# Kernel tuning notes

Measured on AMD Instinct MI355X. Metric: run time of the kernel, lower is better.

## Reference

```python
import jax, jax.numpy as jnp
import numpy as np
import math

NHID = 32
FEAT_SIZE = 32
FEAT_SIZE_LIST = [16, 32, 32, 32]
SEQ_LEN = len(FEAT_SIZE_LIST)   # 4
N_EDGE_LABELS = 3
NLAYERS = 2
N_GRAPHS = 64
FINAL = SEQ_LEN * NHID          # 128


def _pos_enc(max_len, dim):
    pe = np.zeros((max_len, dim), dtype=np.float32)
    pos = np.arange(max_len, dtype=np.float32)[:, None]
    div = np.exp(np.arange(0, dim, 2, dtype=np.float32) * (-math.log(10000.0) / dim))
    pe[:, 0::2] = np.sin(pos * div)
    pe[:, 1::2] = np.cos(pos * div)
    return jnp.asarray(pe)


def _feature_attention(x, wqkv, w1, b1, w2, b2):
    # x: [N, S*NHID] -> attention over the S feature 'tokens' per node
    N, D = x.shape
    S = D // NHID
    xr = x.reshape(N, S, NHID)
    qkv = jnp.einsum('nsf,fh->nsh', xr, wqkv)          # [N,S,3*NHID]
    q, k, v = jnp.split(qkv, 3, axis=-1)
    att = jax.nn.softmax(jnp.einsum('nsh,nth->nst', q, k) / jnp.sqrt(jnp.asarray(NHID, x.dtype)), axis=-1)
    y = jnp.einsum('nst,nth->nsh', att, v)             # [N,S,NHID]
    y = y + (jax.nn.relu(y @ w1 + b1) @ w2 + b2)       # residual FFN
    return y.reshape(N, -1)


def setup_inputs() -> dict:
    key = jax.random.key(0)
    ks = jax.random.split(key, 16)
    N = 100000
    E = 800000
    inp = {
        'x': jax.random.normal(ks[0], (N, 112), dtype=jnp.float32),
        'edge_index0': jax.random.randint(ks[1], (2, E), 0, N),
        'edge_index1': jax.random.randint(ks[2], (2, E), 0, N),
        'edge_index2': jax.random.randint(ks[3], (2, E), 0, N),
        'batch': jnp.sort(jax.random.randint(ks[4], (N,), 0, N_GRAPHS)),
    }
    s = 0.05
    # FeatureLinear encoder (bias-free)
    inp['W_emb'] = jax.random.normal(ks[5], (FEAT_SIZE, NHID), dtype=jnp.float32) * s
    # Per layer: [root, conv0, conv1, conv2] FeatureAttention params, stacked
    A = 1 + N_EDGE_LABELS
    inp['qkv'] = jax.random.normal(ks[6], (NLAYERS, A, NHID, 3 * NHID), dtype=jnp.float32) * s
    inp['ffn_w1'] = jax.random.normal(ks[7], (NLAYERS, A, NHID, NHID), dtype=jnp.float32) * s
    inp['ffn_b1'] = jnp.zeros((NLAYERS, A, NHID), dtype=jnp.float32)
    inp['ffn_w2'] = jax.random.normal(ks[8], (NLAYERS, A, NHID, NHID), dtype=jnp.float32) * s
    inp['ffn_b2'] = jnp.zeros((NLAYERS, A, NHID), dtype=jnp.float32)
    # Heuristic decoder MLP: 128 -> 128 -> 1
    inp['mlp_w1'] = jax.random.normal(ks[9], (FINAL, FINAL), dtype=jnp.float32) * s
    inp['mlp_b1'] = jnp.zeros((FINAL,), dtype=jnp.float32)
    inp['mlp_w2'] = jax.random.normal(ks[10], (FINAL, 1), dtype=jnp.float32) * s
    inp['mlp_b2'] = jnp.zeros((1,), dtype=jnp.float32)
    return inp


def reference(x, edge_index0, edge_index1, edge_index2, batch,
              W_emb, qkv, ffn_w1, ffn_b1, ffn_w2, ffn_b2,
              mlp_w1, mlp_b1, mlp_w2, mlp_b2):
    N = x.shape[0]
    edge_indices = [edge_index0, edge_index1, edge_index2]

    # padding: split by feat_size_list, right-pad each chunk to FEAT_SIZE
    offs = np.cumsum(FEAT_SIZE_LIST)[:-1].tolist()
    chunks = jnp.split(x, offs, axis=1)
    padded = [jnp.pad(c, ((0, 0), (0, FEAT_SIZE - c.shape[1]))) for c in chunks]
    h = jnp.concatenate(padded, axis=1)                       # [N, SEQ_LEN*FEAT_SIZE]

    # sinusoidal positional encoding over the SEQ_LEN feature tokens
    pe = _pos_enc(10, FEAT_SIZE)[:SEQ_LEN]                    # [SEQ_LEN, FEAT_SIZE]
    h = (h.reshape(N, SEQ_LEN, FEAT_SIZE) + pe[None]).reshape(N, -1)

    # FeatureLinear encoder: per-token linear FEAT_SIZE -> NHID
    h = jnp.einsum('nsf,fh->nsh', h.reshape(N, SEQ_LEN, FEAT_SIZE), W_emb).reshape(N, -1)

    # RGNN layers: root attention + per-edge-label attention->scatter-sum
    for l in range(NLAYERS):
        x_out = _feature_attention(h, qkv[l, 0], ffn_w1[l, 0], ffn_b1[l, 0], ffn_w2[l, 0], ffn_b2[l, 0])
        for e in range(N_EDGE_LABELS):
            a = e + 1
            xt = _feature_attention(h, qkv[l, a], ffn_w1[l, a], ffn_b1[l, a], ffn_w2[l, a], ffn_b2[l, a])
            src, dst = edge_indices[e][0], edge_indices[e][1]
            x_out = x_out + jax.ops.segment_sum(xt[src], dst, num_segments=N)
        h = jax.nn.relu(x_out)

    # global mean pool over graphs
    sums = jax.ops.segment_sum(h, batch, num_segments=N_GRAPHS)
    cnts = jax.ops.segment_sum(jnp.ones((N,), h.dtype), batch, num_segments=N_GRAPHS)
    g = sums / jnp.maximum(cnts, 1.0)[:, None]                # [G, FINAL]

    # heuristic decoder
    out = jax.nn.relu(g @ mlp_w1 + mlp_b1) @ mlp_w2 + mlp_b2  # [G, 1]
    return out.squeeze(1)                                     # [G]
```

## Files before the change

kernel.cpp:

```cpp
#include <hip/hip_runtime.h>
#include <hip/hip_bf16.h>
#include <cstdint>
#include <cstddef>


typedef __attribute__((ext_vector_type(8))) short bf16x8;
typedef __attribute__((ext_vector_type(4))) float f32x4;
typedef __attribute__((ext_vector_type(2))) float f32x2;

#if defined(__has_builtin)
#if __has_builtin(__builtin_amdgcn_cvt_pk_fp8_f32) && __has_builtin(__builtin_amdgcn_cvt_pk_f32_fp8)
#define HW_FP8 1
#endif
#endif

__device__ inline short f2bf(float f) {
    union { float f; unsigned u; } v; v.f = f;
    unsigned r = (v.u + 0x7FFFu + ((v.u >> 16) & 1u)) >> 16;
    return (short)r;
}
__device__ inline float bf2f(unsigned short b) {
    union { unsigned u; float f; } v; v.u = ((unsigned)b) << 16;
    return v.f;
}
__device__ inline unsigned pk2(float a, float b) {
    unsigned ua = __float_as_uint(a) + 0x8000u;
    unsigned ub = __float_as_uint(b) + 0x8000u;
    return __builtin_amdgcn_perm(ub, ua, 0x07060302u);
}

#ifndef HW_FP8
__device__ inline unsigned char f2fp8_sw(float f) {
    unsigned s = (__float_as_uint(f) >> 31) & 1u;
    float a = fminf(fabsf(f), 448.f);
    unsigned char bits;
    if (a < 0.015625f) {
        bits = (unsigned char)__float2int_rn(a * 512.f);
    } else {
        int e; float m = frexpf(a, &e);
        int mf = __float2int_rn(m * 16.f);
        if (mf == 16) { mf = 8; e += 1; }
        int ef = e - 1 + 7;
        if (ef > 15) { ef = 15; mf = 14; }
        bits = (unsigned char)((ef << 3) | (mf & 7));
    }
    return (unsigned char)((s << 7) | bits);
}
__device__ inline float fp82f_sw(unsigned b) {
    int s = (b >> 7) & 1, e = (b >> 3) & 15, m = b & 7;
    float v = e ? ldexpf((float)(8 + m), e - 10) : ldexpf((float)m, -9);
    return s ? -v : v;
}
#endif

__device__ inline unsigned pk4fp8(float v0, float v1, float v2, float v3) {
#ifdef HW_FP8
    int w = __builtin_amdgcn_cvt_pk_fp8_f32(v0, v1, 0, false);
    w = __builtin_amdgcn_cvt_pk_fp8_f32(v2, v3, w, true);
    return (unsigned)w;
#else
    return (unsigned)f2fp8_sw(v0) | ((unsigned)f2fp8_sw(v1) << 8) |
           ((unsigned)f2fp8_sw(v2) << 16) | ((unsigned)f2fp8_sw(v3) << 24);
#endif
}

__device__ inline void acc8(float* a, uint2 v) {
#ifdef HW_FP8
    f32x2 f0 = __builtin_amdgcn_cvt_pk_f32_fp8((int)v.x, false);
    f32x2 f1 = __builtin_amdgcn_cvt_pk_f32_fp8((int)v.x, true);
    f32x2 f2 = __builtin_amdgcn_cvt_pk_f32_fp8((int)v.y, false);
    f32x2 f3 = __builtin_amdgcn_cvt_pk_f32_fp8((int)v.y, true);
    a[0] += f0[0]; a[1] += f0[1]; a[2] += f1[0]; a[3] += f1[1];
    a[4] += f2[0]; a[5] += f2[1]; a[6] += f3[0]; a[7] += f3[1];
#else
    unsigned b0 = v.x, b1 = v.y;
#pragma unroll
    for (int j = 0; j < 4; ++j) a[j]     += fp82f_sw((b0 >> (8 * j)) & 0xffu);
#pragma unroll
    for (int j = 0; j < 4; ++j) a[4 + j] += fp82f_sw((b1 >> (8 * j)) & 0xffu);
#endif
}
__device__ inline void acc16(float* a, uint4 v) {
    acc8(a,     make_uint2(v.x, v.y));
    acc8(a + 8, make_uint2(v.z, v.w));
}

__global__ __launch_bounds__(64) void wprep_kernel(
    const float* __restrict__ qkv, const float* __restrict__ fw1,
    const float* __restrict__ fw2, const float* __restrict__ Wemb,
    unsigned short* __restrict__ wpack, float* __restrict__ pwc,
    unsigned char* __restrict__ xtzr,
    int* __restrict__ bcnt, int* __restrict__ gres,
    float* __restrict__ gsum, float* __restrict__ gcnt)
{
    const int pi = blockIdx.x;
    const int lane = threadIdx.x;
    const int gid = pi * 64 + lane;
    for (int i = gid; i < 256; i += 512) { bcnt[i] = 0; gres[i] = 0; }
    for (int i = gid; i < 64 * 128; i += 512) gsum[i] = 0.f;
    if (gid < 64) gcnt[gid] = 0.f;
    if (gid < 32) ((int*)xtzr)[gid] = 0;

    const int q = lane >> 4, m = lane & 15;
    const float* Wq = qkv + (size_t)pi * 32 * 96;
    const float* W1 = fw1 + (size_t)pi * 32 * 32;
    const float* W2 = fw2 + (size_t)pi * 32 * 32;
    unsigned short* dst = wpack + (size_t)pi * 10 * 64 * 8;
#pragma unroll
    for (int ci = 0; ci < 6; ++ci)
#pragma unroll
        for (int j = 0; j < 8; ++j)
            dst[(ci * 64 + lane) * 8 + j] =
                (unsigned short)f2bf(Wq[(q * 8 + j) * 96 + ci * 16 + m]);
#pragma unroll
    for (int t = 0; t < 2; ++t)
#pragma unroll
        for (int j = 0; j < 8; ++j) {
            dst[((6 + t) * 64 + lane) * 8 + j] =
                (unsigned short)f2bf(W1[(q * 8 + j) * 32 + t * 16 + m]);
            dst[((8 + t) * 64 + lane) * 8 + j] =
                (unsigned short)f2bf(W2[(q * 8 + j) * 32 + t * 16 + m]);
        }

    if (pi == 0) {
        const int c = lane & 31;
        for (int ts = lane >> 5; ts < 4; ts += 2) {
            float accp = 0.f;
            for (int f = 0; f < 32; ++f) {
                float div = __expf(-(float)(f & ~1) * (logf(10000.0f) / 32.0f));
                float ang = (float)ts * div;
                float pv = (f & 1) ? cosf(ang) : sinf(ang);
                accp += pv * Wemb[f * 32 + c];
            }
            pwc[ts * 32 + c] = accp;
        }
    }
}

__global__ __launch_bounds__(256) void enc_kernel(
    const float* __restrict__ x, const float* __restrict__ Wemb,
    const float* __restrict__ pwc, unsigned short* __restrict__ h, int N)
{
    __shared__ float sx[64 * 116];
    const int t = threadIdx.x;
    const int nbase = blockIdx.x * 64;

    {
        const float4* xg = (const float4*)x;
        const size_t g4base = ((size_t)nbase * 112) >> 2;
        const size_t lim4 = ((size_t)N * 112) >> 2;
#pragma unroll
        for (int rep = 0; rep < 7; ++rep) {
            int i = t + rep * 256;
            float4 v = make_float4(0.f, 0.f, 0.f, 0.f);
            if (g4base + (size_t)i < lim4) v = xg[g4base + i];
            int row = i / 28;
            int col4 = i - row * 28;
            *(float4*)&sx[row * 116 + col4 * 4] = v;
        }
    }
    __syncthreads();

    const int nl = t >> 2, ts = t & 3;
    const int node = nbase + nl;
    const int offs_[4] = {0, 16, 48, 80};
    const int nv_[4] = {4, 8, 8, 8};
    const int off = offs_[ts];
    const int nv = nv_[ts];

    float xr[32];
#pragma unroll
    for (int j = 0; j < 8; ++j) {
        float4 v = make_float4(0.f, 0.f, 0.f, 0.f);
        if (j < nv) v = *(const float4*)&sx[nl * 116 + off + 4 * j];
        *(float4*)&xr[4 * j] = v;
    }

    float acc[32];
    {
        const float4* pw4 = (const float4*)(pwc + ts * 32);
#pragma unroll
        for (int j = 0; j < 8; ++j) *(float4*)&acc[4 * j] = pw4[j];
    }

#pragma unroll
    for (int f = 0; f < 32; ++f) {
        float xv = xr[f];
#pragma unroll
        for (int c = 0; c < 32; ++c)
            acc[c] = fmaf(xv, Wemb[f * 32 + c], acc[c]);
    }

    if (node < N) {
        unsigned rp[16];
#pragma unroll
        for (int j = 0; j < 16; ++j) rp[j] = pk2(acc[2 * j], acc[2 * j + 1]);
        unsigned short* hp = h + (size_t)node * 128 + ts * 32;
#pragma unroll
        for (int j = 0; j < 4; ++j)
            ((uint4*)hp)[j] = make_uint4(rp[4 * j], rp[4 * j + 1],
                                         rp[4 * j + 2], rp[4 * j + 3]);
    }
}

#define ATT_WAVES 4
#define ULDS 4096
#define WLDS_W (2 * ULDS + 1280)

__global__ __launch_bounds__(256, 4) void attn4_kernel(
    const unsigned short* __restrict__ in,
    unsigned short* __restrict__ outR, unsigned char* __restrict__ out3,
    const unsigned short* __restrict__ wpack,
    const float* __restrict__ fb1, const float* __restrict__ fb2,
    int pibase, int N)
{
    __shared__ char smem[ATT_WAVES * WLDS_W];
    const int lane = threadIdx.x & 63;
    const int wave = threadIdx.x >> 6;
    const int q = lane >> 4;
    const int m = lane & 15;

    char* wb0 = smem + wave * WLDS_W;
    short* Pb = (short*)(wb0 + 2 * ULDS);

    {
        int* p32 = (int*)Pb;
        for (int i = lane; i < 320; i += 64) p32[i] = 0;
    }

    const f32x4 zf = {0.f, 0.f, 0.f, 0.f};
    const int pi = pibase + wave;
    unsigned char* out8 = out3 + (size_t)(wave - 1) * N * 128;

    bf16x8 wqkv[6], w1f[2], w2f[2];
    float b1r[2][4], b2r[2][4];
    {
        const unsigned short* wp = wpack + ((size_t)pi * 10 * 64 + lane) * 8;
#pragma unroll
        for (int ci = 0; ci < 6; ++ci)
            wqkv[ci] = *(const bf16x8*)(wp + ci * 64 * 8);
#pragma unroll
        for (int t = 0; t < 2; ++t) {
            w1f[t] = *(const bf16x8*)(wp + (6 + t) * 64 * 8);
            w2f[t] = *(const bf16x8*)(wp + (8 + t) * 64 * 8);
#pragma unroll
            for (int r = 0; r < 4; ++r) {
                b1r[t][r] = fb1[pi * 32 + 16 * t + q * 4 + r];
                b2r[t][r] = fb2[pi * 32 + 16 * t + q * 4 + r];
            }
        }
    }

    const int nsuper = (N + 7) >> 3;
    for (int stile = blockIdx.x; stile < nsuper; stile += gridDim.x) {
        const int n0 = stile * 8;

        bf16x8 ax[2];
#pragma unroll
        for (int u = 0; u < 2; ++u) {
            bf16x8 a = {0, 0, 0, 0, 0, 0, 0, 0};
            int nm = n0 + 4 * u + (m >> 2);
            if (nm < N)
                a = *(const bf16x8*)(in + (size_t)(n0 + 4 * u) * 128 + m * 32 + q * 8);
            ax[u] = a;
        }

#pragma unroll
        for (int u = 0; u < 2; ++u) {
            char* wbu = wb0 + u * ULDS;
            short* Qb = (short*)(wbu);
            short* Kb = (short*)(wbu + 1280);
            short* VT = (short*)(wbu + 2560);

            f32x4 aQ[2], aK[2], aV[2];
            __builtin_amdgcn_s_setprio(1);
#pragma unroll
            for (int t = 0; t < 2; ++t) {
                aQ[t] = __builtin_amdgcn_mfma_f32_16x16x32_bf16(wqkv[t],     ax[u], zf, 0, 0, 0);
                aK[t] = __builtin_amdgcn_mfma_f32_16x16x32_bf16(wqkv[2 + t], ax[u], zf, 0, 0, 0);
                aV[t] = __builtin_amdgcn_mfma_f32_16x16x32_bf16(ax[u], wqkv[4 + t], zf, 0, 0, 0);
            }
            __builtin_amdgcn_s_setprio(0);
#pragma unroll
            for (int t = 0; t < 2; ++t) {
                uint2 dq, dk, dv;
                dq.x = pk2(aQ[t][0], aQ[t][1]); dq.y = pk2(aQ[t][2], aQ[t][3]);
                dk.x = pk2(aK[t][0], aK[t][1]); dk.y = pk2(aK[t][2], aK[t][3]);
                dv.x = pk2(aV[t][0], aV[t][1]); dv.y = pk2(aV[t][2], aV[t][3]);
                *(uint2*)(Qb + m * 40 + 16 * t + q * 4) = dq;
                *(uint2*)(Kb + m * 40 + 16 * t + q * 4) = dk;
                *(uint2*)(VT + (16 * t + m) * 24 + q * 4) = dv;
            }

            bf16x8 aKf = *(const bf16x8*)(Kb + m * 40 + q * 8);
            bf16x8 bQf = *(const bf16x8*)(Qb + m * 40 + q * 8);
            __builtin_amdgcn_s_setprio(1);
            f32x4 st = __builtin_amdgcn_mfma_f32_16x16x32_bf16(aKf, bQf, zf, 0, 0, 0);
            __builtin_amdgcn_s_setprio(0);

            float v0 = st[0] * 0.1767766952966369f;
            float v1 = st[1] * 0.1767766952966369f;
            float v2 = st[2] * 0.1767766952966369f;
            float v3 = st[3] * 0.1767766952966369f;
            float mx = fmaxf(fmaxf(v0, v1), fmaxf(v2, v3));
            float e0 = __expf(v0 - mx), e1 = __expf(v1 - mx);
            float e2 = __expf(v2 - mx), e3 = __expf(v3 - mx);
            float inv = 1.0f / (e0 + e1 + e2 + e3);
            if (q == (m >> 2)) {
                uint2 dp;
                dp.x = pk2(e0 * inv, e1 * inv);
                dp.y = pk2(e2 * inv, e3 * inv);
                *(uint2*)(Pb + m * 40 + q * 4) = dp;
            }

            f32x4 y[2];
            {
                bf16x8 aVf0 = {0,0,0,0,0,0,0,0}, aVf1 = {0,0,0,0,0,0,0,0};
                bf16x8 bPf  = {0,0,0,0,0,0,0,0};
                if (q < 2) {
                    aVf0 = *(const bf16x8*)(VT + (m) * 24 + q * 8);
                    aVf1 = *(const bf16x8*)(VT + (16 + m) * 24 + q * 8);
                    bPf  = *(const bf16x8*)(Pb + m * 40 + q * 8);
                }
                __builtin_amdgcn_s_setprio(1);
                y[0] = __builtin_amdgcn_mfma_f32_16x16x32_bf16(aVf0, bPf, zf, 0, 0, 0);
                y[1] = __builtin_amdgcn_mfma_f32_16x16x32_bf16(aVf1, bPf, zf, 0, 0, 0);
                __builtin_amdgcn_s_setprio(0);
            }
#pragma unroll
            for (int t = 0; t < 2; ++t) {
                uint2 dy;
                dy.x = pk2(y[t][0], y[t][1]); dy.y = pk2(y[t][2], y[t][3]);
                *(uint2*)(Qb + m * 40 + 16 * t + q * 4) = dy;
            }

            bf16x8 bY = *(const bf16x8*)(Qb + m * 40 + q * 8);
            f32x4 z1[2];
            __builtin_amdgcn_s_setprio(1);
            z1[0] = __builtin_amdgcn_mfma_f32_16x16x32_bf16(w1f[0], bY, zf, 0, 0, 0);
            z1[1] = __builtin_amdgcn_mfma_f32_16x16x32_bf16(w1f[1], bY, zf, 0, 0, 0);
            __builtin_amdgcn_s_setprio(0);
#pragma unroll
            for (int t = 0; t < 2; ++t) {
                uint2 dz;
                dz.x = pk2(fmaxf(z1[t][0] + b1r[t][0], 0.f),
                           fmaxf(z1[t][1] + b1r[t][1], 0.f));
                dz.y = pk2(fmaxf(z1[t][2] + b1r[t][2], 0.f),
                           fmaxf(z1[t][3] + b1r[t][3], 0.f));
                *(uint2*)(Kb + m * 40 + 16 * t + q * 4) = dz;
            }

            bf16x8 bZ = *(const bf16x8*)(Kb + m * 40 + q * 8);
            f32x4 o[2];
            __builtin_amdgcn_s_setprio(1);
            o[0] = __builtin_amdgcn_mfma_f32_16x16x32_bf16(w2f[0], bZ, zf, 0, 0, 0);
            o[1] = __builtin_amdgcn_mfma_f32_16x16x32_bf16(w2f[1], bZ, zf, 0, 0, 0);
            __builtin_amdgcn_s_setprio(0);

            if (n0 + 4 * u + (m >> 2) < N) {
                if (wave == 0) {
#pragma unroll
                    for (int t = 0; t < 2; ++t) {
                        uint2 dd;
                        dd.x = pk2(y[t][0] + o[t][0] + b2r[t][0],
                                   y[t][1] + o[t][1] + b2r[t][1]);
                        dd.y = pk2(y[t][2] + o[t][2] + b2r[t][2],
                                   y[t][3] + o[t][3] + b2r[t][3]);
                        *(uint2*)(outR + (size_t)(n0 + 4 * u) * 128 + m * 32 + 16 * t + q * 4) = dd;
                    }
                } else {
#pragma unroll
                    for (int t = 0; t < 2; ++t) {
                        unsigned pw8 = pk4fp8(
                            (y[t][0] + o[t][0] + b2r[t][0]) * 16.f,
                            (y[t][1] + o[t][1] + b2r[t][1]) * 16.f,
                            (y[t][2] + o[t][2] + b2r[t][2]) * 16.f,
                            (y[t][3] + o[t][3] + b2r[t][3]) * 16.f);
                        *(unsigned*)(out8 + (size_t)(n0 + 4 * u) * 128 + m * 32 + 16 * t + q * 4) = pw8;
                    }
                }
            }
        }
    }
}

#define PA_CHUNK 4096
#define PA_SHIFT 9
#define PA_MAXB  256
#define HB_K     16

__global__ __launch_bounds__(256) void histB_kernel(
    const int* __restrict__ e0, const int* __restrict__ e1,
    const int* __restrict__ e2, int* __restrict__ bcnt, int E)
{
    __shared__ int lh[PA_MAXB];
    const int lab = blockIdx.y;
    const int* e = (lab == 0) ? e0 : (lab == 1) ? e1 : e2;
    const int t = threadIdx.x;
    for (int i = t; i < PA_MAXB; i += 256) lh[i] = 0;
    __syncthreads();
    const int base = blockIdx.x * 256 * HB_K;
#pragma unroll
    for (int k = 0; k < HB_K; ++k) {
        int i = base + k * 256 + t;
        if (i < E) atomicAdd(&lh[e[E + i] >> PA_SHIFT], 1);
    }
    __syncthreads();
    for (int i = t; i < PA_MAXB; i += 256)
        if (lh[i]) atomicAdd(&bcnt[i], lh[i]);
}

__global__ __launch_bounds__(256) void bscan_kernel(
    const int* __restrict__ bcnt, int* __restrict__ bbase)
{
    __shared__ int sd[PA_MAXB];
    const int t = threadIdx.x;
    sd[t] = bcnt[t];
    __syncthreads();
    int own = sd[t];
    for (int o = 1; o < 256; o <<= 1) {
        int v = (t >= o) ? sd[t - o] : 0;
        __syncthreads();
        sd[t] += v;
        __syncthreads();
    }
    bbase[t] = sd[t] - own;
}

__global__ __launch_bounds__(256) void placeA_kernel(
    const int* __restrict__ e0, const int* __restrict__ e1, const int* __restrict__ e2,
    const int* __restrict__ bbase, int* __restrict__ gres,
    int2* __restrict__ pairs, int E, int N)
{
    __shared__ int2 sStage[PA_CHUNK];
    __shared__ int sCnt[PA_MAXB], sScan[PA_MAXB], sCur[PA_MAXB], sGB[PA_MAXB];

    const int lab = blockIdx.y;
    const int t = threadIdx.x;
    const int base = blockIdx.x * PA_CHUNK;
    const int* e = (lab == 0) ? e0 : (lab == 1) ? e1 : e2;
    const int srcoff = lab * N;
    const int nbins = (N + (1 << PA_SHIFT) - 1) >> PA_SHIFT;

    for (int i = t; i < PA_MAXB; i += 256) { sCnt[i] = 0; sCur[i] = 0; }
    __syncthreads();

    int msrc[16], mdst[16];
    const int cnt_total = min(PA_CHUNK, E - base);
#pragma unroll
    for (int k = 0; k < 16; ++k) {
        int i = base + k * 256 + t;
        if (i < E) {
            msrc[k] = srcoff + e[i];
            int d = e[E + i];
            mdst[k] = d;
            atomicAdd(&sCnt[d >> PA_SHIFT], 1);
        } else mdst[k] = -1;
    }
    __syncthreads();

    sScan[t] = sCnt[t];
    __syncthreads();
    for (int o = 1; o < 256; o <<= 1) {
        int v = (t >= o) ? sScan[t - o] : 0;
        __syncthreads();
        sScan[t] += v;
        __syncthreads();
    }
    if (t < nbins && sCnt[t] > 0)
        sGB[t] = bbase[t] + atomicAdd(&gres[t], sCnt[t]);
    __syncthreads();

#pragma unroll
    for (int k = 0; k < 16; ++k) {
        if (mdst[k] >= 0) {
            int bin = mdst[k] >> PA_SHIFT;
            int r = atomicAdd(&sCur[bin], 1);
            sStage[(sScan[bin] - sCnt[bin]) + r] = make_int2(msrc[k], mdst[k]);
        }
    }
    __syncthreads();

    for (int i = t; i < cnt_total; i += 256) {
        int2 pr = sStage[i];
        int bin = pr.y >> PA_SHIFT;
        pairs[sGB[bin] + (i - (sScan[bin] - sCnt[bin]))] = pr;
    }
}

__global__ __launch_bounds__(512) void placeB_kernel(
    const int2* __restrict__ pairs, const int* __restrict__ bbase,
    const int* __restrict__ bcnt, int* __restrict__ offs,
    int* __restrict__ csr, int N, int nbins)
{
    __shared__ int sCnt[512], sScan[512], sFill[512];
    const int bin = blockIdx.x;
    const int t = threadIdx.x;
    const int n0 = bin << PA_SHIFT;
    const int n1 = min(n0 + 512, N);
    const int len = n1 - n0;
    const int rb  = bbase[bin];
    const int cnt = bcnt[bin];
    const int2* gp = pairs + rb;

    sCnt[t] = 0; sFill[t] = 0;
    __syncthreads();
    for (int i = t; i < cnt; i += 512)
        atomicAdd(&sCnt[gp[i].y - n0], 1);
    __syncthreads();
    sScan[t] = sCnt[t];
    __syncthreads();
    for (int o = 1; o < 512; o <<= 1) {
        int v = (t >= o) ? sScan[t - o] : 0;
        __syncthreads();
        sScan[t] += v;
        __syncthreads();
    }
    const int excl = sScan[t] - sCnt[t];
    if (t < len) offs[n0 + t] = rb + excl;
    if (bin == nbins - 1 && t == 0) offs[N] = rb + cnt;
    sScan[t] = excl;
    __syncthreads();

    for (int i = t; i < cnt; i += 512) {
        int2 pr = gp[i];
        int ln = pr.y - n0;
        int p = atomicAdd(&sFill[ln], 1);
        csr[rb + sScan[ln] + p] = pr.x;
    }
}

__global__ __launch_bounds__(256) void agg3_kernel(
    const unsigned short* __restrict__ xtR,
    const unsigned char* __restrict__ xt3,
    const int* __restrict__ csr, const int* __restrict__ offs,
    unsigned short* __restrict__ hout, int N)
{
    const int wv = threadIdx.x >> 6, lane = threadIdx.x & 63;
    const int oct = lane >> 3;
    const int fl  = lane & 7;
    const int dst = blockIdx.x * 32 + wv * 8 + oct;
    const int ZR  = 3 * N;
    const unsigned fb = (unsigned)fl << 4;

    const int beg = offs[min(dst, N)];
    const int end = offs[min(dst + 1, N)];
    const int last = end - 1;

    const unsigned short* rp = xtR + (size_t)min(dst, N - 1) * 128 + fl * 16;
    bf16x8 rv0 = *(const bf16x8*)(rp);
    bf16x8 rv1 = *(const bf16x8*)(rp + 8);

    float a[16];
#pragma unroll
    for (int i = 0; i < 16; ++i) a[i] = 0.f;

    int k = beg;
    int c0, c1, c2, c3;
    {
        int i0 = csr[k], i1 = csr[k + 1], i2 = csr[k + 2], i3 = csr[k + 3];
        c0 = (k     > last) ? ZR : i0;
        c1 = (k + 1 > last) ? ZR : i1;
        c2 = (k + 2 > last) ? ZR : i2;
        c3 = (k + 3 > last) ? ZR : i3;
    }

    while (__any(k < end)) {
        uint4 v0 = *(const uint4*)(xt3 + (((unsigned)c0) << 7) + fb);
        uint4 v1 = *(const uint4*)(xt3 + (((unsigned)c1) << 7) + fb);
        uint4 v2 = *(const uint4*)(xt3 + (((unsigned)c2) << 7) + fb);
        uint4 v3 = *(const uint4*)(xt3 + (((unsigned)c3) << 7) + fb);
        int kn = min(k + 4, end);
        int j0 = csr[kn], j1 = csr[kn + 1], j2 = csr[kn + 2], j3 = csr[kn + 3];
        c0 = (kn     > last) ? ZR : j0;
        c1 = (kn + 1 > last) ? ZR : j1;
        c2 = (kn + 2 > last) ? ZR : j2;
        c3 = (kn + 3 > last) ? ZR : j3;
        acc16(a, v0);
        acc16(a, v1);
        acc16(a, v2);
        acc16(a, v3);
        k = kn;
    }

    if (dst < N) {
        unsigned r[8];
#pragma unroll
        for (int t = 0; t < 4; ++t) {
            float f0 = bf2f((unsigned short)rv0[2 * t])     + 0.0625f * a[2 * t];
            float f1 = bf2f((unsigned short)rv0[2 * t + 1]) + 0.0625f * a[2 * t + 1];
            r[t] = pk2(fmaxf(f0, 0.f), fmaxf(f1, 0.f));
        }
#pragma unroll
        for (int t = 0; t < 4; ++t) {
            float f0 = bf2f((unsigned short)rv1[2 * t])     + 0.0625f * a[8 + 2 * t];
            float f1 = bf2f((unsigned short)rv1[2 * t + 1]) + 0.0625f * a[8 + 2 * t + 1];
            r[4 + t] = pk2(fmaxf(f0, 0.f), fmaxf(f1, 0.f));
        }
        unsigned short* hp = hout + (size_t)dst * 128 + fl * 16;
        *(uint4*)hp       = make_uint4(r[0], r[1], r[2], r[3]);
        *(uint4*)(hp + 8) = make_uint4(r[4], r[5], r[6], r[7]);
    }
}

__global__ __launch_bounds__(256) void pool_kernel(
    const unsigned short* __restrict__ in, const int* __restrict__ batch,
    float* __restrict__ gsum, float* __restrict__ gcnt, int N)
{
    int t = threadIdx.x;
    int j = t & 127, half = t >> 7;
    int n0 = blockIdx.x * 64 + half * 32;
    float acc = 0.f, c = 0.f; int cur = -1;
    for (int i = 0; i < 32; ++i) {
        int n = n0 + i;
        if (n >= N) break;
        int g = batch[n];
        if (g != cur) {
            if (cur >= 0) {
                atomicAdd(&gsum[cur * 128 + j], acc);
                if (j == 0) atomicAdd(&gcnt[cur], c);
            }
            cur = g; acc = 0.f; c = 0.f;
        }
        acc += bf2f(in[(size_t)n * 128 + j]);
        c += 1.f;
    }
    if (cur >= 0) {
        atomicAdd(&gsum[cur * 128 + j], acc);
        if (j == 0) atomicAdd(&gcnt[cur], c);
    }
}

__global__ __launch_bounds__(128) void dec_kernel(
    const float* __restrict__ gsum, const float* __restrict__ gcnt,
    const float* __restrict__ W1, const float* __restrict__ B1,
    const float* __restrict__ W2, const float* __restrict__ B2,
    float* __restrict__ out)
{
    __shared__ float sg[128];
    __shared__ float sh[128];
    int t = threadIdx.x, b = blockIdx.x;
    float cinv = 1.0f / fmaxf(gcnt[b], 1.0f);
    sg[t] = gsum[b * 128 + t] * cinv;
    __syncthreads();
    float acc = B1[t];
    for (int f = 0; f < 128; ++f) acc += sg[f] * W1[f * 128 + t];
    sh[t] = fmaxf(acc, 0.f) * W2[t];
    __syncthreads();
    for (int o = 64; o > 0; o >>= 1) {
        if (t < o) sh[t] += sh[t + o];
        __syncthreads();
    }
    if (t == 0) out[b] = sh[0] + B2[0];
}

extern "C" void kernel_launch(void* const* d_in, const int* in_sizes, int n_in,
                              void* d_out, int out_size, void* d_ws, size_t ws_size,
                              hipStream_t stream)
{
    const float* x    = (const float*)d_in[0];
    const int*   e0   = (const int*)d_in[1];
    const int*   e1   = (const int*)d_in[2];
    const int*   e2   = (const int*)d_in[3];
    const int*   bat  = (const int*)d_in[4];
    const float* Wemb = (const float*)d_in[5];
    const float* qkv  = (const float*)d_in[6];
    const float* fw1  = (const float*)d_in[7];
    const float* fb1  = (const float*)d_in[8];
    const float* fw2  = (const float*)d_in[9];
    const float* fb2  = (const float*)d_in[10];
    const float* mw1  = (const float*)d_in[11];
    const float* mb1  = (const float*)d_in[12];
    const float* mw2  = (const float*)d_in[13];
    const float* mb2  = (const float*)d_in[14];
    const int N = in_sizes[0] / 112;
    const int E = in_sizes[1] / 2;
    float* outp = (float*)d_out;
    (void)n_in; (void)out_size; (void)ws_size;

    char* w = (char*)d_ws;
    auto alloc = [&](size_t bytes) {
        char* p = w; w += (bytes + 255) & ~(size_t)255; return p;
    };
    unsigned short* h0    = (unsigned short*)alloc((size_t)N * 128 * 2);
    unsigned short* h1    = (unsigned short*)alloc((size_t)N * 128 * 2);
    unsigned short* xtR   = (unsigned short*)alloc((size_t)N * 128 * 2);
    unsigned char*  xt3   = (unsigned char*)alloc((size_t)3 * N * 128 + 128);
    unsigned short* wpack = (unsigned short*)alloc(8 * 10 * 64 * 8 * 2);
    float* pwc   = (float*)alloc(128 * 4);
    int*   csr   = (int*)alloc((size_t)3 * E * 4 + 64);
    int*   offs  = (int*)alloc((size_t)(N + 1) * 4);
    int*   bcnt  = (int*)alloc(PA_MAXB * 4);
    int*   bbase = (int*)alloc(PA_MAXB * 4);
    int*   gres  = (int*)alloc(PA_MAXB * 4);
    float* gsum  = (float*)alloc(64 * 128 * 4);
    float* gcnt  = (float*)alloc(64 * 4);
    int2* pairs = (int2*)xtR;
    unsigned char* xtzr = xt3 + (size_t)3 * N * 128;

    const int nbins = (N + (1 << PA_SHIFT) - 1) >> PA_SHIFT;

    wprep_kernel<<<8, 64, 0, stream>>>(qkv, fw1, fw2, Wemb, wpack, pwc, xtzr,
                                       bcnt, gres, gsum, gcnt);
    enc_kernel<<<(N + 63) / 64, 256, 0, stream>>>(x, Wemb, pwc, h0, N);

    histB_kernel<<<dim3((E + 256 * HB_K - 1) / (256 * HB_K), 3), 256, 0, stream>>>(
        e0, e1, e2, bcnt, E);
    bscan_kernel<<<1, 256, 0, stream>>>(bcnt, bbase);
    placeA_kernel<<<dim3((E + PA_CHUNK - 1) / PA_CHUNK, 3), 256, 0, stream>>>(
        e0, e1, e2, bbase, gres, pairs, E, N);
    placeB_kernel<<<nbins, 512, 0, stream>>>(pairs, bbase, bcnt, offs, csr, N, nbins);

    const int ATT_GRID = 1024;
    auto run_layer = [&](const unsigned short* lin, unsigned short* lout, int l) {
        attn4_kernel<<<ATT_GRID, 256, 0, stream>>>(
            lin, xtR, xt3, wpack, fb1, fb2, l * 4, N);
        agg3_kernel<<<(N + 31) / 32, 256, 0, stream>>>(xtR, xt3, csr, offs, lout, N);
    };
    run_layer(h0, h1, 0);
    run_layer(h1, h0, 1);

    pool_kernel<<<(N + 63) / 64, 256, 0, stream>>>(h0, bat, gsum, gcnt, N);
    dec_kernel<<<64, 128, 0, stream>>>(gsum, gcnt, mw1, mb1, mw2, mb2, outp);
}
```

Measured before the change: 450.1 us.

## Interleave two attention sub-tiles stage by stage and drop separate P buffer

The attention kernel now runs each stage (QKV projection, scores/softmax, PV, FFN1, FFN2) for both 4-node sub-tiles before moving to the next stage. This gives independent MFMA and LDS work between dependent steps to hide latency. The separate zero-initialised P buffer is removed: probabilities go into the now-free Q region after zeroing it, and loads are made unconditional with a register-level zero mask. LDS per block shrinks, but register pressure rises because y is kept for both sub-tiles.

```diff
diff --git a/kernel.cpp b/kernel.cpp
--- a/kernel.cpp
+++ b/kernel.cpp
@@ -205,7 +205,6 @@
 
 #define ATT_WAVES 4
 #define ULDS 4096
-#define WLDS_W (2 * ULDS + 1280)
 
 __global__ __launch_bounds__(256, 4) void attn4_kernel(
     const unsigned short* __restrict__ in,
@@ -214,19 +213,16 @@
     const float* __restrict__ fb1, const float* __restrict__ fb2,
     int pibase, int N)
 {
-    __shared__ char smem[ATT_WAVES * WLDS_W];
+    __shared__ char smem[ATT_WAVES * 2 * ULDS];
     const int lane = threadIdx.x & 63;
     const int wave = threadIdx.x >> 6;
     const int q = lane >> 4;
     const int m = lane & 15;
 
-    char* wb0 = smem + wave * WLDS_W;
-    short* Pb = (short*)(wb0 + 2 * ULDS);
-
-    {
-        int* p32 = (int*)Pb;
-        for (int i = lane; i < 320; i += 64) p32[i] = 0;
-    }
+    char* wb0 = smem + wave * (2 * ULDS);
+    short* Qb[2] = {(short*)(wb0),        (short*)(wb0 + ULDS)};
+    short* Kb[2] = {(short*)(wb0 + 1280), (short*)(wb0 + ULDS + 1280)};
+    short* VT[2] = {(short*)(wb0 + 2560), (short*)(wb0 + ULDS + 2560)};
 
     const f32x4 zf = {0.f, 0.f, 0.f, 0.f};
     const int pi = pibase + wave;
@@ -265,13 +261,10 @@
             ax[u] = a;
         }
 
+        f32x4 y[2][2];
+
 #pragma unroll
         for (int u = 0; u < 2; ++u) {
-            char* wbu = wb0 + u * ULDS;
-            short* Qb = (short*)(wbu);
-            short* Kb = (short*)(wbu + 1280);
-            short* VT = (short*)(wbu + 2560);
-
             f32x4 aQ[2], aK[2], aV[2];
             __builtin_amdgcn_s_setprio(1);
 #pragma unroll
@@ -287,13 +280,16 @@
                 dq.x = pk2(aQ[t][0], aQ[t][1]); dq.y = pk2(aQ[t][2], aQ[t][3]);
                 dk.x = pk2(aK[t][0], aK[t][1]); dk.y = pk2(aK[t][2], aK[t][3]);
                 dv.x = pk2(aV[t][0], aV[t][1]); dv.y = pk2(aV[t][2], aV[t][3]);
-                *(uint2*)(Qb + m * 40 + 16 * t + q * 4) = dq;
-                *(uint2*)(Kb + m * 40 + 16 * t + q * 4) = dk;
-                *(uint2*)(VT + (16 * t + m) * 24 + q * 4) = dv;
-            }
-
-            bf16x8 aKf = *(const bf16x8*)(Kb + m * 40 + q * 8);
-            bf16x8 bQf = *(const bf16x8*)(Qb + m * 40 + q * 8);
+                *(uint2*)(Qb[u] + m * 40 + 16 * t + q * 4) = dq;
+                *(uint2*)(Kb[u] + m * 40 + 16 * t + q * 4) = dk;
+                *(uint2*)(VT[u] + (16 * t + m) * 24 + q * 4) = dv;
+            }
+        }
+
+#pragma unroll
+        for (int u = 0; u < 2; ++u) {
+            bf16x8 aKf = *(const bf16x8*)(Kb[u] + m * 40 + q * 8);
+            bf16x8 bQf = *(const bf16x8*)(Qb[u] + m * 40 + q * 8);
             __builtin_amdgcn_s_setprio(1);
             f32x4 st = __builtin_amdgcn_mfma_f32_16x16x32_bf16(aKf, bQf, zf, 0, 0, 0);
             __builtin_amdgcn_s_setprio(0);
@@ -306,35 +302,43 @@
             float e0 = __expf(v0 - mx), e1 = __expf(v1 - mx);
             float e2 = __expf(v2 - mx), e3 = __expf(v3 - mx);
             float inv = 1.0f / (e0 + e1 + e2 + e3);
+
+            *(uint2*)(Qb[u] + (lane >> 2) * 40 + (lane & 3) * 4) =
+                make_uint2(0u, 0u);
             if (q == (m >> 2)) {
                 uint2 dp;
                 dp.x = pk2(e0 * inv, e1 * inv);
                 dp.y = pk2(e2 * inv, e3 * inv);
-                *(uint2*)(Pb + m * 40 + q * 4) = dp;
-            }
-
-            f32x4 y[2];
-            {
-                bf16x8 aVf0 = {0,0,0,0,0,0,0,0}, aVf1 = {0,0,0,0,0,0,0,0};
-                bf16x8 bPf  = {0,0,0,0,0,0,0,0};
-                if (q < 2) {
-                    aVf0 = *(const bf16x8*)(VT + (m) * 24 + q * 8);
-                    aVf1 = *(const bf16x8*)(VT + (16 + m) * 24 + q * 8);
-                    bPf  = *(const bf16x8*)(Pb + m * 40 + q * 8);
-                }
-                __builtin_amdgcn_s_setprio(1);
-                y[0] = __builtin_amdgcn_mfma_f32_16x16x32_bf16(aVf0, bPf, zf, 0, 0, 0);
-                y[1] = __builtin_amdgcn_mfma_f32_16x16x32_bf16(aVf1, bPf, zf, 0, 0, 0);
-                __builtin_amdgcn_s_setprio(0);
-            }
+                *(uint2*)(Qb[u] + m * 40 + q * 4) = dp;
+            }
+        }
+
+#pragma unroll
+        for (int u = 0; u < 2; ++u) {
+            const int qv = q & 1;
+            bf16x8 aVf0 = *(const bf16x8*)(VT[u] + m * 24 + qv * 8);
+            bf16x8 aVf1 = *(const bf16x8*)(VT[u] + (16 + m) * 24 + qv * 8);
+            bf16x8 bPf  = *(const bf16x8*)(Qb[u] + m * 40 + qv * 8);
+            if (q >= 2) {
+                const bf16x8 zb = {0, 0, 0, 0, 0, 0, 0, 0};
+                aVf0 = zb; aVf1 = zb; bPf = zb;
+            }
+            __builtin_amdgcn_s_setprio(1);
+            y[u][0] = __builtin_amdgcn_mfma_f32_16x16x32_bf16(aVf0, bPf, zf, 0, 0, 0);
+            y[u][1] = __builtin_amdgcn_mfma_f32_16x16x32_bf16(aVf1, bPf, zf, 0, 0, 0);
+            __builtin_amdgcn_s_setprio(0);
 #pragma unroll
             for (int t = 0; t < 2; ++t) {
                 uint2 dy;
-                dy.x = pk2(y[t][0], y[t][1]); dy.y = pk2(y[t][2], y[t][3]);
-                *(uint2*)(Qb + m * 40 + 16 * t + q * 4) = dy;
-            }
-
-            bf16x8 bY = *(const bf16x8*)(Qb + m * 40 + q * 8);
+                dy.x = pk2(y[u][t][0], y[u][t][1]);
+                dy.y = pk2(y[u][t][2], y[u][t][3]);
+                *(uint2*)(Qb[u] + m * 40 + 16 * t + q * 4) = dy;
+            }
+        }
+
+#pragma unroll
+        for (int u = 0; u < 2; ++u) {
+            bf16x8 bY = *(const bf16x8*)(Qb[u] + m * 40 + q * 8);
             f32x4 z1[2];
             __builtin_amdgcn_s_setprio(1);
             z1[0] = __builtin_amdgcn_mfma_f32_16x16x32_bf16(w1f[0], bY, zf, 0, 0, 0);
@@ -347,10 +351,13 @@
                            fmaxf(z1[t][1] + b1r[t][1], 0.f));
                 dz.y = pk2(fmaxf(z1[t][2] + b1r[t][2], 0.f),
                            fmaxf(z1[t][3] + b1r[t][3], 0.f));
-                *(uint2*)(Kb + m * 40 + 16 * t + q * 4) = dz;
-            }
-
-            bf16x8 bZ = *(const bf16x8*)(Kb + m * 40 + q * 8);
+                *(uint2*)(Kb[u] + m * 40 + 16 * t + q * 4) = dz;
+            }
+        }
+
+#pragma unroll
+        for (int u = 0; u < 2; ++u) {
+            bf16x8 bZ = *(const bf16x8*)(Kb[u] + m * 40 + q * 8);
             f32x4 o[2];
             __builtin_amdgcn_s_setprio(1);
             o[0] = __builtin_amdgcn_mfma_f32_16x16x32_bf16(w2f[0], bZ, zf, 0, 0, 0);
@@ -362,20 +369,20 @@
 #pragma unroll
                     for (int t = 0; t < 2; ++t) {
                         uint2 dd;
-                        dd.x = pk2(y[t][0] + o[t][0] + b2r[t][0],
-                                   y[t][1] + o[t][1] + b2r[t][1]);
-                        dd.y = pk2(y[t][2] + o[t][2] + b2r[t][2],
-                                   y[t][3] + o[t][3] + b2r[t][3]);
+                        dd.x = pk2(y[u][t][0] + o[t][0] + b2r[t][0],
+                                   y[u][t][1] + o[t][1] + b2r[t][1]);
+                        dd.y = pk2(y[u][t][2] + o[t][2] + b2r[t][2],
+                                   y[u][t][3] + o[t][3] + b2r[t][3]);
                         *(uint2*)(outR + (size_t)(n0 + 4 * u) * 128 + m * 32 + 16 * t + q * 4) = dd;
                     }
                 } else {
 #pragma unroll
                     for (int t = 0; t < 2; ++t) {
                         unsigned pw8 = pk4fp8(
-                            (y[t][0] + o[t][0] + b2r[t][0]) * 16.f,
-                            (y[t][1] + o[t][1] + b2r[t][1]) * 16.f,
-                            (y[t][2] + o[t][2] + b2r[t][2]) * 16.f,
-                            (y[t][3] + o[t][3] + b2r[t][3]) * 16.f);
+                            (y[u][t][0] + o[t][0] + b2r[t][0]) * 16.f,
+                            (y[u][t][1] + o[t][1] + b2r[t][1]) * 16.f,
+                            (y[u][t][2] + o[t][2] + b2r[t][2]) * 16.f,
+                            (y[u][t][3] + o[t][3] + b2r[t][3]) * 16.f);
                         *(unsigned*)(out8 + (size_t)(n0 + 4 * u) * 128 + m * 32 + 16 * t + q * 4) = pw8;
                     }
                 }
```

Measured after the change: 455.5 us. About the same (+1.2%).
